# Kernel optimization log

Hardware: AMD Instinct MI355X
Metric: run time of the kernel (lower is better)

Reference implementation:

```python
import jax, jax.numpy as jnp
import numpy as np

L, N1, N2 = 2, 2, 2
E1 = sum(1 + i for i in range(N1))      # 3 first-stage DAG edges per layer
E2 = sum(N1 + i for i in range(N2))     # 5 last-stage DAG edges per layer
DIM, IN_DIM, NUM_CLASSES = 256, 128, 10
N_NODES, N_EDGES, N_GRAPHS = 8000, 128000, 64


def setup_inputs():
    key = jax.random.key(0)
    ks = jax.random.split(key, 16)
    s = 0.05  # weight scale to keep activations bounded through stacked cells
    return {
        'h': jax.random.normal(ks[0], (N_NODES, IN_DIM), jnp.float32),
        'W_emb': jax.random.normal(ks[1], (IN_DIM, DIM), jnp.float32) * s,
        'b_emb': jnp.zeros((DIM,), jnp.float32),
        'Wf_dense': jax.random.normal(ks[2], (L, E1, DIM, DIM), jnp.float32) * s,
        'bf_dense': jnp.zeros((L, E1, DIM), jnp.float32),
        'Wf_sparse': jax.random.normal(ks[3], (L, E1, DIM, DIM), jnp.float32) * s,
        'bf_sparse': jnp.zeros((L, E1, DIM), jnp.float32),
        'Wl_dense': jax.random.normal(ks[4], (L, E2, DIM, DIM), jnp.float32) * s,
        'bl_dense': jnp.zeros((L, E2, DIM), jnp.float32),
        'Wl_sparse': jax.random.normal(ks[5], (L, E2, DIM, DIM), jnp.float32) * s,
        'bl_sparse': jnp.zeros((L, E2, DIM), jnp.float32),
        'a_first': 0.001 * jax.random.normal(ks[6], (L * E1, 4), jnp.float32),
        'a_mid': 0.001 * jax.random.normal(ks[7], (L * N1, 4), jnp.float32),
        'a_last': 0.001 * jax.random.normal(ks[8], (L * E2, 4), jnp.float32),
        'C1': jax.random.normal(ks[9], (DIM, DIM // 2), jnp.float32) * s,
        'c1b': jnp.zeros((DIM // 2,), jnp.float32),
        'C2': jax.random.normal(ks[10], (DIM // 2, DIM // 4), jnp.float32) * s,
        'c2b': jnp.zeros((DIM // 4,), jnp.float32),
        'C3': jax.random.normal(ks[11], (DIM // 4, NUM_CLASSES), jnp.float32) * s,
        'c3b': jnp.zeros((NUM_CLASSES,), jnp.float32),
        'src': jax.random.randint(ks[12], (N_EDGES,), 0, N_NODES, jnp.int32),
        'dst': jax.random.randint(ks[13], (N_EDGES,), 0, N_NODES, jnp.int32),
        'graph_ids': jnp.sort(jax.random.randint(ks[14], (N_NODES,), 0, N_GRAPHS, jnp.int32)),
        'num_graphs': N_GRAPHS,
    }


def forward(h, W_emb, b_emb, Wf_dense, bf_dense, Wf_sparse, bf_sparse,
            Wl_dense, bl_dense, Wl_sparse, bl_sparse, a_first, a_mid, a_last,
            C1, c1b, C2, c2b, C3, c3b, src, dst, graph_ids, num_graphs):
    N = h.shape[0]
    deg0 = jax.ops.segment_sum(jnp.ones((src.shape[0],), h.dtype), dst, num_segments=N)
    deg = jnp.maximum(deg0, 1.0)[:, None]      # in-degree, clamped for mean
    has_nb = (deg0 > 0)[:, None]

    # DARTS softmax over candidate ops (per DAG edge)
    wf = jax.nn.softmax(a_first, axis=1)
    wm = jax.nn.softmax(a_mid, axis=1)
    wl = jax.nn.softmax(a_last, axis=1)

    def mixed(xj, w, Wd, bd, Ws, bs):
        # mixture over {f_zero, f_identity, f_dense, f_sparse}
        dense = xj @ Wd + bd
        agg = jax.ops.segment_sum(xj[src], dst, num_segments=N) / deg  # mean msg-passing
        sparse = agg @ Ws + bs
        return w[1] * xj + w[2] * dense + w[3] * sparse  # w[0]*zero omitted

    x = h @ W_emb + b_emb  # embedding (Linear, data_type='gc')
    for l in range(L):
        # first stage: DAG over N1 intermediate nodes
        states = [x]
        e = 0
        for n in range(1, N1 + 1):
            s = jnp.zeros_like(x)
            for j in range(n):
                s = s + mixed(states[j], wf[l * E1 + e], Wf_dense[l, e], bf_dense[l, e],
                              Wf_sparse[l, e], bf_sparse[l, e])
                e += 1
            states.append(jax.nn.relu(s))
        # middle stage: mixture over {identity, max, mean, sum} neighbor aggregators
        mids = []
        for n in range(N1):
            xn = states[n + 1]
            w = wm[l * N1 + n]
            msg = xn[src]
            msum = jax.ops.segment_sum(msg, dst, num_segments=N)
            mmean = msum / deg
            mmax = jnp.where(has_nb, jax.ops.segment_max(msg, dst, num_segments=N), 0.0)
            mids.append(w[0] * xn + w[1] * mmax + w[2] * mmean + w[3] * msum)
        # last stage: DAG over N2 output nodes, inputs = middle states + prior lasts
        lasts = []
        e = 0
        for n in range(N2):
            ins = mids + lasts
            s = jnp.zeros_like(x)
            for j in range(N1 + n):
                s = s + mixed(ins[j], wl[l * E2 + e], Wl_dense[l, e], bl_dense[l, e],
                              Wl_sparse[l, e], bl_sparse[l, e])
                e += 1
            lasts.append(jax.nn.relu(s))
        x = x + sum(lasts) / float(N2)  # residual cell output

    # dgl.mean_nodes readout: per-graph mean over nodes
    cnt = jnp.maximum(jax.ops.segment_sum(jnp.ones((N,), x.dtype), graph_ids,
                                          num_segments=num_graphs), 1.0)[:, None]
    hg = jax.ops.segment_sum(x, graph_ids, num_segments=num_graphs) / cnt
    # MLPReadout: 256 -> 128 -> 64 -> 10
    y = jax.nn.relu(hg @ C1 + c1b)
    y = jax.nn.relu(y @ C2 + c2b)
    return y @ C3 + c3b


def reference(h, W_emb, b_emb, Wf_dense, bf_dense, Wf_sparse, bf_sparse,
              Wl_dense, bl_dense, Wl_sparse, bl_sparse, a_first, a_mid, a_last,
              C1, c1b, C2, c2b, C3, c3b, src, dst, graph_ids, num_graphs):
    return forward(h, W_emb, b_emb, Wf_dense, bf_dense, Wf_sparse, bf_sparse,
                   Wl_dense, bl_dense, Wl_sparse, bl_sparse, a_first, a_mid, a_last,
                   C1, c1b, C2, c2b, C3, c3b, src, dst, graph_ids, num_graphs)
```

## Files before the change

### kernel.cpp

```cpp
#include <hip/hip_runtime.h>

#define N_NODES   8000
#define M_PAD     8192
#define N_EDGES   128000
#define N_GRAPHS  64
#define DIM       256
#define IN_DIM    128

typedef short bf16x8 __attribute__((ext_vector_type(8)));
typedef float f32x4 __attribute__((ext_vector_type(4)));

static __device__ __forceinline__ float bf2f(unsigned v) {
  return __uint_as_float(v << 16);
}
static __device__ __forceinline__ unsigned f2bf(float f) {
  unsigned u = __float_as_uint(f);
  return (u + 0x7fffu + ((u >> 16) & 1u)) >> 16;
}

__global__ __launch_bounds__(256) void k_count(const int* __restrict__ dst,
                                               int* __restrict__ counts) {
  int e = blockIdx.x * 256 + threadIdx.x;
  if (e < N_EDGES) atomicAdd(&counts[dst[e]], 1);
}

__global__ __launch_bounds__(256) void k_scan(const int* __restrict__ counts,
                                              int* __restrict__ row_ofs,
                                              int* __restrict__ cursor,
                                              float* __restrict__ invdeg) {
  __shared__ int chunk[256];
  const int per = (N_NODES + 255) / 256;
  int t = threadIdx.x;
  int base = t * per;
  int s = 0;
  for (int i = 0; i < per; ++i) {
    int idx = base + i;
    if (idx < N_NODES) s += counts[idx];
  }
  chunk[t] = s;
  __syncthreads();
  for (int off = 1; off < 256; off <<= 1) {
    int v = 0;
    if (t >= off) v = chunk[t - off];
    __syncthreads();
    if (t >= off) chunk[t] += v;
    __syncthreads();
  }
  int run = (t > 0) ? chunk[t - 1] : 0;
  for (int i = 0; i < per; ++i) {
    int idx = base + i;
    if (idx < N_NODES) {
      row_ofs[idx] = run;
      cursor[idx] = run;
      int c = counts[idx];
      invdeg[idx] = 1.0f / (float)(c > 1 ? c : 1);
      run += c;
    }
  }
  if (t == 0) row_ofs[N_NODES] = chunk[255];
}

__global__ __launch_bounds__(256) void k_fill(const int* __restrict__ src,
                                              const int* __restrict__ dst,
                                              int* __restrict__ cursor,
                                              int* __restrict__ csr_src) {
  int e = blockIdx.x * 256 + threadIdx.x;
  if (e < N_EDGES) {
    int p = atomicAdd(&cursor[dst[e]], 1);
    csr_src[p] = src[e];
  }
}

__global__ __launch_bounds__(64) void k_softmax(const float* __restrict__ af,
                                                const float* __restrict__ am,
                                                const float* __restrict__ al,
                                                float* __restrict__ w) {
  int t = threadIdx.x;
  const float* sp;
  float* dp;
  if (t < 6)       { sp = af + t * 4;        dp = w + t * 4; }
  else if (t < 10) { sp = am + (t - 6) * 4;  dp = w + 24 + (t - 6) * 4; }
  else if (t < 20) { sp = al + (t - 10) * 4; dp = w + 40 + (t - 10) * 4; }
  else return;
  float a0 = sp[0], a1 = sp[1], a2 = sp[2], a3 = sp[3];
  float m = fmaxf(fmaxf(a0, a1), fmaxf(a2, a3));
  float e0 = expf(a0 - m), e1 = expf(a1 - m), e2 = expf(a2 - m), e3 = expf(a3 - m);
  float si = 1.0f / (e0 + e1 + e2 + e3);
  dp[0] = e0 * si; dp[1] = e1 * si; dp[2] = e2 * si; dp[3] = e3 * si;
}

__global__ __launch_bounds__(256) void k_cvt_bf16(const float* __restrict__ in,
                                                  unsigned short* __restrict__ out,
                                                  int n) {
  int i = blockIdx.x * 256 + threadIdx.x;
  if (i < n) out[i] = (unsigned short)f2bf(in[i]);
}

__global__ __launch_bounds__(256) void k_transpose_cvt(const float* __restrict__ in,
                                                       unsigned short* __restrict__ out,
                                                       int K, int N) {
  __shared__ float tile[32][33];
  int k0 = blockIdx.x * 32, n0 = blockIdx.y * 32;
  int tx = threadIdx.x & 31, ty = threadIdx.x >> 5;
#pragma unroll
  for (int i = 0; i < 4; ++i)
    tile[ty + 8 * i][tx] = in[(size_t)(k0 + ty + 8 * i) * N + n0 + tx];
  __syncthreads();
#pragma unroll
  for (int i = 0; i < 4; ++i)
    out[(size_t)(n0 + ty + 8 * i) * K + k0 + tx] =
        (unsigned short)f2bf(tile[tx][ty + 8 * i]);
}

__global__ __launch_bounds__(256) void k_transpose_cvt32(const float* __restrict__ Wfd,
                                                         const float* __restrict__ Wfs,
                                                         const float* __restrict__ Wld,
                                                         const float* __restrict__ Wls,
                                                         const float* __restrict__ wsoft,
                                                         unsigned short* __restrict__ out) {
  __shared__ float tile[32][33];
  int z = blockIdx.z;
  const float* in;
  float coef;
  const float* wf = wsoft;
  const float* wl = wsoft + 40;
  if (z < 6)       { in = Wfd + (size_t)z * DIM * DIM;        coef = wf[z * 4 + 2]; }
  else if (z < 12) { in = Wfs + (size_t)(z - 6) * DIM * DIM;  coef = wf[(z - 6) * 4 + 3]; }
  else if (z < 22) { in = Wld + (size_t)(z - 12) * DIM * DIM; coef = wl[(z - 12) * 4 + 2]; }
  else             { in = Wls + (size_t)(z - 22) * DIM * DIM; coef = wl[(z - 22) * 4 + 3]; }
  unsigned short* o = out + (size_t)z * DIM * DIM;
  int k0 = blockIdx.x * 32, n0 = blockIdx.y * 32;
  int tx = threadIdx.x & 31, ty = threadIdx.x >> 5;
#pragma unroll
  for (int i = 0; i < 4; ++i)
    tile[ty + 8 * i][tx] = in[(size_t)(k0 + ty + 8 * i) * DIM + n0 + tx];
  __syncthreads();
#pragma unroll
  for (int i = 0; i < 4; ++i)
    o[(size_t)(n0 + ty + 8 * i) * DIM + k0 + tx] =
        (unsigned short)f2bf(coef * tile[tx][ty + 8 * i]);
}

#define SEG_ACC(u) \
  { s0 += bf2f((u).x & 0xffffu); s1 += bf2f((u).x >> 16); \
    s2 += bf2f((u).y & 0xffffu); s3 += bf2f((u).y >> 16); }

__global__ __launch_bounds__(256) void k_segmean_bf(const unsigned short* __restrict__ X,
                                                    const int* __restrict__ row_ofs,
                                                    const int* __restrict__ csr_src,
                                                    const float* __restrict__ invdeg,
                                                    unsigned short* __restrict__ out) {
  int node = blockIdx.x * 4 + (threadIdx.x >> 6);
  int l = threadIdx.x & 63;
  if (node >= N_NODES) return;
  int beg = row_ofs[node], end = row_ofs[node + 1];
  float s0 = 0.f, s1 = 0.f, s2 = 0.f, s3 = 0.f;
  int e = beg;
  for (; e + 4 <= end; e += 4) {
    int i0 = csr_src[e], i1 = csr_src[e + 1], i2 = csr_src[e + 2], i3 = csr_src[e + 3];
    uint2 u0 = *(const uint2*)&X[(size_t)i0 * DIM + 4 * l];
    uint2 u1 = *(const uint2*)&X[(size_t)i1 * DIM + 4 * l];
    uint2 u2 = *(const uint2*)&X[(size_t)i2 * DIM + 4 * l];
    uint2 u3 = *(const uint2*)&X[(size_t)i3 * DIM + 4 * l];
    SEG_ACC(u0) SEG_ACC(u1) SEG_ACC(u2) SEG_ACC(u3)
  }
  for (; e < end; ++e) {
    uint2 u = *(const uint2*)&X[(size_t)csr_src[e] * DIM + 4 * l];
    SEG_ACC(u)
  }
  float iv = invdeg[node];
  uint2 o;
  o.x = f2bf(s0 * iv) | (f2bf(s1 * iv) << 16);
  o.y = f2bf(s2 * iv) | (f2bf(s3 * iv) << 16);
  *(uint2*)&out[(size_t)node * DIM + 4 * l] = o;
}

__global__ __launch_bounds__(256) void k_segmean2_bf(const unsigned short* __restrict__ X0,
                                                     const unsigned short* __restrict__ X1,
                                                     const int* __restrict__ row_ofs,
                                                     const int* __restrict__ csr_src,
                                                     const float* __restrict__ invdeg,
                                                     unsigned short* __restrict__ out0,
                                                     unsigned short* __restrict__ out1) {
  int node = blockIdx.x * 4 + (threadIdx.x >> 6);
  int l = threadIdx.x & 63;
  if (node >= N_NODES) return;
  int beg = row_ofs[node], end = row_ofs[node + 1];
  float a0 = 0.f, a1 = 0.f, a2 = 0.f, a3 = 0.f;
  float b0 = 0.f, b1 = 0.f, b2 = 0.f, b3 = 0.f;
  int e = beg;
  for (; e + 2 <= end; e += 2) {
    size_t r0 = (size_t)csr_src[e] * DIM + 4 * l;
    size_t r1 = (size_t)csr_src[e + 1] * DIM + 4 * l;
    uint2 u0 = *(const uint2*)&X0[r0];
    uint2 v0 = *(const uint2*)&X1[r0];
    uint2 u1 = *(const uint2*)&X0[r1];
    uint2 v1 = *(const uint2*)&X1[r1];
    a0 += bf2f(u0.x & 0xffffu) + bf2f(u1.x & 0xffffu);
    a1 += bf2f(u0.x >> 16) + bf2f(u1.x >> 16);
    a2 += bf2f(u0.y & 0xffffu) + bf2f(u1.y & 0xffffu);
    a3 += bf2f(u0.y >> 16) + bf2f(u1.y >> 16);
    b0 += bf2f(v0.x & 0xffffu) + bf2f(v1.x & 0xffffu);
    b1 += bf2f(v0.x >> 16) + bf2f(v1.x >> 16);
    b2 += bf2f(v0.y & 0xffffu) + bf2f(v1.y & 0xffffu);
    b3 += bf2f(v0.y >> 16) + bf2f(v1.y >> 16);
  }
  for (; e < end; ++e) {
    size_t rb = (size_t)csr_src[e] * DIM + 4 * l;
    uint2 u = *(const uint2*)&X0[rb];
    uint2 v = *(const uint2*)&X1[rb];
    a0 += bf2f(u.x & 0xffffu); a1 += bf2f(u.x >> 16);
    a2 += bf2f(u.y & 0xffffu); a3 += bf2f(u.y >> 16);
    b0 += bf2f(v.x & 0xffffu); b1 += bf2f(v.x >> 16);
    b2 += bf2f(v.y & 0xffffu); b3 += bf2f(v.y >> 16);
  }
  float iv = invdeg[node];
  uint2 o;
  o.x = f2bf(a0 * iv) | (f2bf(a1 * iv) << 16);
  o.y = f2bf(a2 * iv) | (f2bf(a3 * iv) << 16);
  *(uint2*)&out0[(size_t)node * DIM + 4 * l] = o;
  o.x = f2bf(b0 * iv) | (f2bf(b1 * iv) << 16);
  o.y = f2bf(b2 * iv) | (f2bf(b3 * iv) << 16);
  *(uint2*)&out1[(size_t)node * DIM + 4 * l] = o;
}

__global__ __launch_bounds__(256) void k_segmid_bf(const unsigned short* __restrict__ Xn,
                                                   const int* __restrict__ row_ofs,
                                                   const int* __restrict__ csr_src,
                                                   const float* __restrict__ invdeg,
                                                   const float* __restrict__ wrow,
                                                   unsigned short* __restrict__ mean_out,
                                                   unsigned short* __restrict__ mids_out) {
  int node = blockIdx.x * 4 + (threadIdx.x >> 6);
  int l = threadIdx.x & 63;
  if (node >= N_NODES) return;
  int beg = row_ofs[node], end = row_ofs[node + 1];
  float s0 = 0.f, s1 = 0.f, s2 = 0.f, s3 = 0.f;
  float m0 = 0.f, m1 = 0.f, m2 = 0.f, m3 = 0.f;
  int e = beg;
  for (; e + 4 <= end; e += 4) {
    int i0 = csr_src[e], i1 = csr_src[e + 1], i2 = csr_src[e + 2], i3 = csr_src[e + 3];
    uint2 u0 = *(const uint2*)&Xn[(size_t)i0 * DIM + 4 * l];
    uint2 u1 = *(const uint2*)&Xn[(size_t)i1 * DIM + 4 * l];
    uint2 u2 = *(const uint2*)&Xn[(size_t)i2 * DIM + 4 * l];
    uint2 u3 = *(const uint2*)&Xn[(size_t)i3 * DIM + 4 * l];
#pragma unroll
    for (int j = 0; j < 4; ++j) {
      uint2 u = (j == 0) ? u0 : (j == 1) ? u1 : (j == 2) ? u2 : u3;
      float v0 = bf2f(u.x & 0xffffu), v1 = bf2f(u.x >> 16);
      float v2 = bf2f(u.y & 0xffffu), v3 = bf2f(u.y >> 16);
      s0 += v0; s1 += v1; s2 += v2; s3 += v3;
      m0 = fmaxf(m0, v0); m1 = fmaxf(m1, v1);
      m2 = fmaxf(m2, v2); m3 = fmaxf(m3, v3);
    }
  }
  for (; e < end; ++e) {
    uint2 u = *(const uint2*)&Xn[(size_t)csr_src[e] * DIM + 4 * l];
    float v0 = bf2f(u.x & 0xffffu), v1 = bf2f(u.x >> 16);
    float v2 = bf2f(u.y & 0xffffu), v3 = bf2f(u.y >> 16);
    s0 += v0; s1 += v1; s2 += v2; s3 += v3;
    m0 = fmaxf(m0, v0); m1 = fmaxf(m1, v1);
    m2 = fmaxf(m2, v2); m3 = fmaxf(m3, v3);
  }
  float iv = invdeg[node];
  float e0 = s0 * iv, e1 = s1 * iv, e2 = s2 * iv, e3 = s3 * iv;
  if (mean_out) {
    uint2 o;
    o.x = f2bf(e0) | (f2bf(e1) << 16);
    o.y = f2bf(e2) | (f2bf(e3) << 16);
    *(uint2*)&mean_out[(size_t)node * DIM + 4 * l] = o;
  }
  float w0 = wrow[0], w1 = wrow[1], w2 = wrow[2], w3 = wrow[3];
  uint2 xu = *(const uint2*)&Xn[(size_t)node * DIM + 4 * l];
  float x0 = bf2f(xu.x & 0xffffu), x1 = bf2f(xu.x >> 16);
  float x2 = bf2f(xu.y & 0xffffu), x3 = bf2f(xu.y >> 16);
  uint2 o;
  o.x = f2bf(w0 * x0 + w1 * m0 + w2 * e0 + w3 * s0) |
        (f2bf(w0 * x1 + w1 * m1 + w2 * e1 + w3 * s1) << 16);
  o.y = f2bf(w0 * x2 + w1 * m2 + w2 * e2 + w3 * s2) |
        (f2bf(w0 * x3 + w1 * m3 + w2 * e3 + w3 * s3) << 16);
  *(uint2*)&mids_out[(size_t)node * DIM + 4 * l] = o;
}

struct GemmDescB {
  const unsigned short* A[6];
  const unsigned short* W[6];
  const float* b[6];
  const float* c[6];
  const unsigned short* I[3];
  const float* ic[3];
  const float* resid;
  const unsigned short* addl;
  float* out_f32;
  unsigned short* out_bf;
  int nmat, nid, K, relu;
};

__global__ __launch_bounds__(256) void k_gemm_mfma(GemmDescB d) {
  __shared__ __align__(16) unsigned short As[2][64][72];
  __shared__ __align__(16) unsigned short Bs[2][64][72];
  const int tid = threadIdx.x;
  const int b = blockIdx.x;
  const int bm = ((b & 7) + 8 * (b >> 5)) * 64;
  const int bn = ((b >> 3) & 3) * 64;
  const int w = tid >> 6, l = tid & 63;
  const int wm = (w >> 1) * 32, wn = (w & 1) * 32;
  const int lr = l & 15, lk = (l >> 4) * 8;
  const int ldr = tid >> 3, ldk = (tid & 7) * 8;

  const int K = d.K;
  const int kds = (K == 256) ? 2 : 1;
  const int kmask = (1 << kds) - 1;
  const int nsteps = d.nmat << kds;

  f32x4 zero = {0.f, 0.f, 0.f, 0.f};
  f32x4 acc[2][2];
  acc[0][0] = zero; acc[0][1] = zero; acc[1][0] = zero; acc[1][1] = zero;

  auto gload = [&](int s, uint4& a0, uint4& a1, uint4& b0, uint4& b1) {
    int t = s >> kds;
    int k0 = (s & kmask) << 6;
    const unsigned short* __restrict__ A = d.A[t];
    const unsigned short* __restrict__ W = d.W[t];
    a0 = *(const uint4*)&A[(size_t)(bm + ldr) * K + k0 + ldk];
    a1 = *(const uint4*)&A[(size_t)(bm + ldr + 32) * K + k0 + ldk];
    b0 = *(const uint4*)&W[(size_t)(bn + ldr) * K + k0 + ldk];
    b1 = *(const uint4*)&W[(size_t)(bn + ldr + 32) * K + k0 + ldk];
  };

  {
    uint4 a0, a1, b0, b1;
    gload(0, a0, a1, b0, b1);
    *(uint4*)&As[0][ldr][ldk] = a0;
    *(uint4*)&As[0][ldr + 32][ldk] = a1;
    *(uint4*)&Bs[0][ldr][ldk] = b0;
    *(uint4*)&Bs[0][ldr + 32][ldk] = b1;
  }
  __syncthreads();

  int buf = 0;
  for (int s = 0; s < nsteps; ++s) {
    uint4 na0, na1, nb0, nb1;
    const bool more = (s + 1 < nsteps);
    if (more) gload(s + 1, na0, na1, nb0, nb1);
#pragma unroll
    for (int ks = 0; ks < 2; ++ks) {
      bf16x8 a0 = *(const bf16x8*)&As[buf][wm + lr][ks * 32 + lk];
      bf16x8 a1 = *(const bf16x8*)&As[buf][wm + 16 + lr][ks * 32 + lk];
      bf16x8 b0 = *(const bf16x8*)&Bs[buf][wn + lr][ks * 32 + lk];
      bf16x8 b1 = *(const bf16x8*)&Bs[buf][wn + 16 + lr][ks * 32 + lk];
      acc[0][0] = __builtin_amdgcn_mfma_f32_16x16x32_bf16(a0, b0, acc[0][0], 0, 0, 0);
      acc[0][1] = __builtin_amdgcn_mfma_f32_16x16x32_bf16(a0, b1, acc[0][1], 0, 0, 0);
      acc[1][0] = __builtin_amdgcn_mfma_f32_16x16x32_bf16(a1, b0, acc[1][0], 0, 0, 0);
      acc[1][1] = __builtin_amdgcn_mfma_f32_16x16x32_bf16(a1, b1, acc[1][1], 0, 0, 0);
    }
    if (more) {
      *(uint4*)&As[buf ^ 1][ldr][ldk] = na0;
      *(uint4*)&As[buf ^ 1][ldr + 32][ldk] = na1;
      *(uint4*)&Bs[buf ^ 1][ldr][ldk] = nb0;
      *(uint4*)&Bs[buf ^ 1][ldr + 32][ldk] = nb1;
    }
    __syncthreads();
    buf ^= 1;
  }

  float bias[2] = {0.f, 0.f};
  for (int t = 0; t < d.nmat; ++t) {
    if (d.b[t]) {
      float c = d.c[t] ? *d.c[t] : 1.0f;
      bias[0] += c * d.b[t][bn + wn + lr];
      bias[1] += c * d.b[t][bn + wn + 16 + lr];
    }
  }
  float vout[2][2][4];
#pragma unroll
  for (int m = 0; m < 2; ++m)
#pragma unroll
    for (int n = 0; n < 2; ++n)
#pragma unroll
      for (int i = 0; i < 4; ++i) vout[m][n][i] = acc[m][n][i] + bias[n];
#pragma unroll
  for (int u = 0; u < 3; ++u) {
    if (u < d.nid) {
      float icu = *d.ic[u];
      const unsigned short* __restrict__ I = d.I[u];
#pragma unroll
      for (int m = 0; m < 2; ++m)
#pragma unroll
        for (int n = 0; n < 2; ++n)
#pragma unroll
          for (int i = 0; i < 4; ++i) {
            int row = bm + wm + m * 16 + (l >> 4) * 4 + i;
            int col = bn + wn + n * 16 + lr;
            vout[m][n][i] += icu * bf2f(I[(size_t)row * DIM + col]);
          }
    }
  }
#pragma unroll
  for (int m = 0; m < 2; ++m)
#pragma unroll
    for (int n = 0; n < 2; ++n)
#pragma unroll
      for (int i = 0; i < 4; ++i) {
        int row = bm + wm + m * 16 + (l >> 4) * 4 + i;
        int col = bn + wn + n * 16 + lr;
        size_t idx = (size_t)row * DIM + col;
        float v = vout[m][n][i];
        if (d.relu) v = fmaxf(v, 0.f);
        if (d.resid) v = d.resid[idx] + 0.5f * (bf2f(d.addl[idx]) + v);
        d.out_bf[idx] = (unsigned short)f2bf(v);
        if (d.out_f32) d.out_f32[idx] = v;
      }
}

__global__ __launch_bounds__(256) void k_readout(const float* __restrict__ x,
                                                 const int* __restrict__ gid,
                                                 float* __restrict__ hg) {
  int g = blockIdx.x, t = threadIdx.x;
  int lo = 0, hi = N_NODES;
  while (lo < hi) { int m = (lo + hi) >> 1; if (gid[m] < g) lo = m + 1; else hi = m; }
  int beg = lo;
  lo = beg; hi = N_NODES;
  while (lo < hi) { int m = (lo + hi) >> 1; if (gid[m] <= g) lo = m + 1; else hi = m; }
  int end = lo;
  float s = 0.f;
  for (int i = beg; i < end; ++i) s += x[(size_t)i * DIM + t];
  int cnt = end - beg;
  hg[g * DIM + t] = s / (float)(cnt > 1 ? cnt : 1);
}

__global__ __launch_bounds__(256) void k_mlp(const float* __restrict__ hg,
                                             const float* __restrict__ C1,
                                             const float* __restrict__ c1b,
                                             const float* __restrict__ C2,
                                             const float* __restrict__ c2b,
                                             const float* __restrict__ C3,
                                             const float* __restrict__ c3b,
                                             float* __restrict__ out) {
  int g = blockIdx.x, t = threadIdx.x;
  __shared__ float h0[256], h1[128], h2[64];
  h0[t] = hg[g * DIM + t];
  __syncthreads();
  if (t < 128) {
    float s = c1b[t];
    for (int k = 0; k < 256; ++k) s = fmaf(h0[k], C1[k * 128 + t], s);
    h1[t] = fmaxf(s, 0.f);
  }
  __syncthreads();
  if (t < 64) {
    float s = c2b[t];
    for (int k = 0; k < 128; ++k) s = fmaf(h1[k], C2[k * 64 + t], s);
    h2[t] = fmaxf(s, 0.f);
  }
  __syncthreads();
  if (t < 10) {
    float s = c3b[t];
    for (int k = 0; k < 64; ++k) s = fmaf(h2[k], C3[k * 10 + t], s);
    out[g * 10 + t] = s;
  }
}

extern "C" void kernel_launch(void* const* d_in, const int* in_sizes, int n_in,
                              void* d_out, int out_size, void* d_ws, size_t ws_size,
                              hipStream_t stream) {
  const float* h     = (const float*)d_in[0];
  const float* W_emb = (const float*)d_in[1];
  const float* b_emb = (const float*)d_in[2];
  const float* Wf_d  = (const float*)d_in[3];
  const float* bf_d  = (const float*)d_in[4];
  const float* Wf_s  = (const float*)d_in[5];
  const float* bf_s  = (const float*)d_in[6];
  const float* Wl_d  = (const float*)d_in[7];
  const float* bl_d  = (const float*)d_in[8];
  const float* Wl_s  = (const float*)d_in[9];
  const float* bl_s  = (const float*)d_in[10];
  const float* a_first = (const float*)d_in[11];
  const float* a_mid   = (const float*)d_in[12];
  const float* a_last  = (const float*)d_in[13];
  const float* C1 = (const float*)d_in[14];
  const float* c1b = (const float*)d_in[15];
  const float* C2 = (const float*)d_in[16];
  const float* c2b = (const float*)d_in[17];
  const float* C3 = (const float*)d_in[18];
  const float* c3b = (const float*)d_in[19];
  const int* src = (const int*)d_in[20];
  const int* dst = (const int*)d_in[21];
  const int* gid = (const int*)d_in[22];
  (void)in_sizes; (void)n_in; (void)out_size; (void)ws_size;

  char* p = (char*)d_ws;
  auto alloc = [&](size_t bytes) {
    void* r = (void*)p;
    p += (bytes + 255) & ~(size_t)255;
    return r;
  };
  typedef unsigned short u16;
  const size_t NBF = (size_t)M_PAD * DIM * sizeof(u16);
  float* x_f32 = (float*)alloc((size_t)M_PAD * DIM * sizeof(float));
  u16* xb    = (u16*)alloc(NBF);
  u16* s1b   = (u16*)alloc(NBF);
  u16* s2b   = (u16*)alloc(NBF);
  u16* m0b   = (u16*)alloc(NBF);
  u16* m1b   = (u16*)alloc(NBF);
  u16* l0b   = (u16*)alloc(NBF);
  u16* aggAb = (u16*)alloc(NBF);
  u16* aggBb = (u16*)alloc(NBF);
  u16* h_bf  = (u16*)alloc((size_t)M_PAD * IN_DIM * sizeof(u16));
  u16* WT    = (u16*)alloc((size_t)(DIM * IN_DIM + 32 * DIM * DIM) * sizeof(u16));
  u16* WTe   = WT;
  u16* WTfd  = WT + DIM * IN_DIM;
  u16* WTfs  = WTfd + 6 * DIM * DIM;
  u16* WTld  = WTfs + 6 * DIM * DIM;
  u16* WTls  = WTld + 10 * DIM * DIM;
  float* invdeg = (float*)alloc(N_NODES * sizeof(float));
  int* counts  = (int*)alloc(N_NODES * sizeof(int));
  int* row_ofs = (int*)alloc((N_NODES + 1) * sizeof(int));
  int* cursor  = (int*)alloc(N_NODES * sizeof(int));
  int* csr_src = (int*)alloc(N_EDGES * sizeof(int));
  float* wsoft = (float*)alloc(80 * sizeof(float));
  float* hg    = (float*)alloc(N_GRAPHS * DIM * sizeof(float));

  const int EB = (N_EDGES + 255) / 256;
  const int PADR = M_PAD - N_NODES;

  hipMemsetAsync(counts, 0, N_NODES * sizeof(int), stream);
  hipMemsetAsync(h_bf + (size_t)N_NODES * IN_DIM, 0, (size_t)PADR * IN_DIM * sizeof(u16), stream);
  hipMemsetAsync(aggAb + (size_t)N_NODES * DIM, 0, (size_t)PADR * DIM * sizeof(u16), stream);
  hipMemsetAsync(aggBb + (size_t)N_NODES * DIM, 0, (size_t)PADR * DIM * sizeof(u16), stream);
  hipMemsetAsync(m0b + (size_t)N_NODES * DIM, 0, (size_t)PADR * DIM * sizeof(u16), stream);
  hipMemsetAsync(m1b + (size_t)N_NODES * DIM, 0, (size_t)PADR * DIM * sizeof(u16), stream);

  k_count<<<EB, 256, 0, stream>>>(dst, counts);
  k_scan<<<1, 256, 0, stream>>>(counts, row_ofs, cursor, invdeg);
  k_fill<<<EB, 256, 0, stream>>>(src, dst, cursor, csr_src);
  k_softmax<<<1, 64, 0, stream>>>(a_first, a_mid, a_last, wsoft);

  const float* wf = wsoft;
  const float* wm = wsoft + 24;
  const float* wl = wsoft + 40;

  k_cvt_bf16<<<(N_NODES * IN_DIM + 255) / 256, 256, 0, stream>>>(h, h_bf, N_NODES * IN_DIM);
  k_transpose_cvt<<<dim3(IN_DIM / 32, DIM / 32, 1), 256, 0, stream>>>(W_emb, WTe, IN_DIM, DIM);
  k_transpose_cvt32<<<dim3(8, 8, 32), 256, 0, stream>>>(Wf_d, Wf_s, Wl_d, Wl_s, wsoft, WTfd);

  const int GG = (M_PAD / 64) * (DIM / 64);
  const int SB = (N_NODES + 3) / 4;

  {
    GemmDescB d{};
    d.A[0] = h_bf; d.W[0] = WTe; d.b[0] = b_emb; d.c[0] = nullptr;
    d.nmat = 1; d.nid = 0; d.K = IN_DIM; d.relu = 0;
    d.out_f32 = x_f32; d.out_bf = xb;
    k_gemm_mfma<<<GG, 256, 0, stream>>>(d);
  }

  for (int l = 0; l < 2; ++l) {
    auto WFD = [&](int e) { return WTfd + (size_t)(l * 3 + e) * DIM * DIM; };
    auto BFD = [&](int e) { return bf_d + (size_t)(l * 3 + e) * DIM; };
    auto WFS = [&](int e) { return WTfs + (size_t)(l * 3 + e) * DIM * DIM; };
    auto BFS = [&](int e) { return bf_s + (size_t)(l * 3 + e) * DIM; };
    auto WLD = [&](int e) { return WTld + (size_t)(l * 5 + e) * DIM * DIM; };
    auto BLD = [&](int e) { return bl_d + (size_t)(l * 5 + e) * DIM; };
    auto WLS = [&](int e) { return WTls + (size_t)(l * 5 + e) * DIM * DIM; };
    auto BLS = [&](int e) { return bl_s + (size_t)(l * 5 + e) * DIM; };
    auto WFrow = [&](int e) { return wf + (l * 3 + e) * 4; };
    auto WMrow = [&](int n) { return wm + (l * 2 + n) * 4; };
    auto WLrow = [&](int e) { return wl + (l * 5 + e) * 4; };

    auto edge = [&](GemmDescB& d, const u16* X, const u16* AG,
                    const u16* Wd, const float* bd,
                    const u16* Ws, const float* bs, const float* wrow) {
      d.A[d.nmat] = X;  d.W[d.nmat] = Wd; d.b[d.nmat] = bd; d.c[d.nmat] = wrow + 2; d.nmat++;
      d.A[d.nmat] = AG; d.W[d.nmat] = Ws; d.b[d.nmat] = bs; d.c[d.nmat] = wrow + 3; d.nmat++;
      d.I[d.nid] = X; d.ic[d.nid] = wrow + 1; d.nid++;
    };

    k_segmean_bf<<<SB, 256, 0, stream>>>(xb, row_ofs, csr_src, invdeg, aggAb);

    {
      GemmDescB d{}; d.K = DIM; d.relu = 1; d.out_bf = s1b;
      edge(d, xb, aggAb, WFD(0), BFD(0), WFS(0), BFS(0), WFrow(0));
      k_gemm_mfma<<<GG, 256, 0, stream>>>(d);
    }

    k_segmid_bf<<<SB, 256, 0, stream>>>(s1b, row_ofs, csr_src, invdeg, WMrow(0), aggBb, m0b);

    {
      GemmDescB d{}; d.K = DIM; d.relu = 1; d.out_bf = s2b;
      edge(d, xb,  aggAb, WFD(1), BFD(1), WFS(1), BFS(1), WFrow(1));
      edge(d, s1b, aggBb, WFD(2), BFD(2), WFS(2), BFS(2), WFrow(2));
      k_gemm_mfma<<<GG, 256, 0, stream>>>(d);
    }

    k_segmid_bf<<<SB, 256, 0, stream>>>(s2b, row_ofs, csr_src, invdeg, WMrow(1), nullptr, m1b);

    k_segmean2_bf<<<SB, 256, 0, stream>>>(m0b, m1b, row_ofs, csr_src, invdeg, aggAb, aggBb);

    {
      GemmDescB d{}; d.K = DIM; d.relu = 1; d.out_bf = l0b;
      edge(d, m0b, aggAb, WLD(0), BLD(0), WLS(0), BLS(0), WLrow(0));
      edge(d, m1b, aggBb, WLD(1), BLD(1), WLS(1), BLS(1), WLrow(1));
      k_gemm_mfma<<<GG, 256, 0, stream>>>(d);
    }

    k_segmean_bf<<<SB, 256, 0, stream>>>(l0b, row_ofs, csr_src, invdeg, s1b);

    {
      GemmDescB d{}; d.K = DIM; d.relu = 1;
      edge(d, m0b, aggAb, WLD(2), BLD(2), WLS(2), BLS(2), WLrow(2));
      edge(d, m1b, aggBb, WLD(3), BLD(3), WLS(3), BLS(3), WLrow(3));
      edge(d, l0b, s1b,   WLD(4), BLD(4), WLS(4), BLS(4), WLrow(4));
      d.resid = x_f32; d.addl = l0b;
      d.out_f32 = x_f32; d.out_bf = xb;
      k_gemm_mfma<<<GG, 256, 0, stream>>>(d);
    }
  }

  k_readout<<<N_GRAPHS, 256, 0, stream>>>(x_f32, gid, hg);
  k_mlp<<<N_GRAPHS, 256, 0, stream>>>(hg, C1, c1b, C2, c2b, C3, c3b, (float*)d_out);
}
```

Before: 361.3 us.

## Share A-operand loads across sibling edge GEMMs via wide-N dual-output tiles

The GEMM kernel can now produce two output halves, each with its own weights, bias and epilogue. Edges that read the same inputs (xb/aggA for first-stage edges 0 and 1, m0/m1 for last-stage edges 0-3) are computed in one wider launch, with the partial sum saved in fp32 and added back later through a new 'pre' term. This stops the later GEMMs from re-reading the shared operands and shrinks their K depth. The cost is extra fp32 partial buffers written and read back. The separate memsets are also merged into a single init kernel.

Result: no change. 359.7 us (-0.4%).

```diff
diff --git a/kernel.cpp b/kernel.cpp
--- a/kernel.cpp
+++ b/kernel.cpp
@@ -2,6 +2,7 @@
 
 #define N_NODES   8000
 #define M_PAD     8192
+#define PADR      (M_PAD - N_NODES)
 #define N_EDGES   128000
 #define N_GRAPHS  64
 #define DIM       256
@@ -16,6 +17,18 @@
 static __device__ __forceinline__ unsigned f2bf(float f) {
   unsigned u = __float_as_uint(f);
   return (u + 0x7fffu + ((u >> 16) & 1u)) >> 16;
+}
+
+__global__ __launch_bounds__(256) void k_init(int* __restrict__ counts,
+                                              unsigned short* __restrict__ hpad,
+                                              unsigned short* __restrict__ p0,
+                                              unsigned short* __restrict__ p1,
+                                              unsigned short* __restrict__ p2,
+                                              unsigned short* __restrict__ p3) {
+  int i = blockIdx.x * 256 + threadIdx.x;
+  if (i < N_NODES) counts[i] = 0;
+  if (i < PADR * IN_DIM) hpad[i] = 0;
+  if (i < PADR * DIM) { p0[i] = 0; p1[i] = 0; p2[i] = 0; p3[i] = 0; }
 }
 
 __global__ __launch_bounds__(256) void k_count(const int* __restrict__ dst,
@@ -282,27 +295,31 @@
   *(uint2*)&mids_out[(size_t)node * DIM + 4 * l] = o;
 }
 
-struct GemmDescB {
-  const unsigned short* A[6];
-  const unsigned short* W[6];
-  const float* b[6];
-  const float* c[6];
-  const unsigned short* I[3];
-  const float* ic[3];
-  const float* resid;
-  const unsigned short* addl;
-  float* out_f32;
-  unsigned short* out_bf;
-  int nmat, nid, K, relu;
+struct GemmDescW {
+  const unsigned short* A[4];
+  const unsigned short* W[2][4];
+  const float* b[2][4];
+  const float* c[2][4];
+  const unsigned short* I[2];
+  const float* ic[2][2];
+  const float* pre[2];
+  const float* resid[2];
+  const unsigned short* addl[2];
+  float* out_f32[2];
+  unsigned short* out_bf[2];
+  int nmat, nid, K, relu[2], colshift;
 };
 
-__global__ __launch_bounds__(256) void k_gemm_mfma(GemmDescB d) {
+__global__ __launch_bounds__(256) void k_gemm_mfma(GemmDescW d) {
   __shared__ __align__(16) unsigned short As[2][64][72];
   __shared__ __align__(16) unsigned short Bs[2][64][72];
   const int tid = threadIdx.x;
   const int b = blockIdx.x;
-  const int bm = ((b & 7) + 8 * (b >> 5)) * 64;
-  const int bn = ((b >> 3) & 3) * 64;
+  const int cs = d.colshift;
+  const int c = (b >> 3) & ((1 << cs) - 1);
+  const int bm = ((b & 7) + 8 * (b >> (3 + cs))) * 64;
+  const int half = c >> 2;
+  const int bn = (c & 3) * 64;
   const int w = tid >> 6, l = tid & 63;
   const int wm = (w >> 1) * 32, wn = (w & 1) * 32;
   const int lr = l & 15, lk = (l >> 4) * 8;
@@ -321,7 +338,7 @@
     int t = s >> kds;
     int k0 = (s & kmask) << 6;
     const unsigned short* __restrict__ A = d.A[t];
-    const unsigned short* __restrict__ W = d.W[t];
+    const unsigned short* __restrict__ W = d.W[half][t];
     a0 = *(const uint4*)&A[(size_t)(bm + ldr) * K + k0 + ldk];
     a1 = *(const uint4*)&A[(size_t)(bm + ldr + 32) * K + k0 + ldk];
     b0 = *(const uint4*)&W[(size_t)(bn + ldr) * K + k0 + ldk];
@@ -366,10 +383,11 @@
 
   float bias[2] = {0.f, 0.f};
   for (int t = 0; t < d.nmat; ++t) {
-    if (d.b[t]) {
-      float c = d.c[t] ? *d.c[t] : 1.0f;
-      bias[0] += c * d.b[t][bn + wn + lr];
-      bias[1] += c * d.b[t][bn + wn + 16 + lr];
+    const float* bp = d.b[half][t];
+    if (bp) {
+      float cc = d.c[half][t] ? *d.c[half][t] : 1.0f;
+      bias[0] += cc * bp[bn + wn + lr];
+      bias[1] += cc * bp[bn + wn + 16 + lr];
     }
   }
   float vout[2][2][4];
@@ -380,9 +398,9 @@
 #pragma unroll
       for (int i = 0; i < 4; ++i) vout[m][n][i] = acc[m][n][i] + bias[n];
 #pragma unroll
-  for (int u = 0; u < 3; ++u) {
+  for (int u = 0; u < 2; ++u) {
     if (u < d.nid) {
-      float icu = *d.ic[u];
+      float icu = *d.ic[half][u];
       const unsigned short* __restrict__ I = d.I[u];
 #pragma unroll
       for (int m = 0; m < 2; ++m)
@@ -396,6 +414,12 @@
           }
     }
   }
+  const float* pre = d.pre[half];
+  const float* resid = d.resid[half];
+  const unsigned short* addl = d.addl[half];
+  unsigned short* obf = d.out_bf[half];
+  float* of32 = d.out_f32[half];
+  const int do_relu = d.relu[half];
 #pragma unroll
   for (int m = 0; m < 2; ++m)
 #pragma unroll
@@ -406,10 +430,11 @@
         int col = bn + wn + n * 16 + lr;
         size_t idx = (size_t)row * DIM + col;
         float v = vout[m][n][i];
-        if (d.relu) v = fmaxf(v, 0.f);
-        if (d.resid) v = d.resid[idx] + 0.5f * (bf2f(d.addl[idx]) + v);
-        d.out_bf[idx] = (unsigned short)f2bf(v);
-        if (d.out_f32) d.out_f32[idx] = v;
+        if (pre) v += pre[idx];
+        if (do_relu) v = fmaxf(v, 0.f);
+        if (resid) v = resid[idx] + 0.5f * (bf2f(addl[idx]) + v);
+        if (obf) obf[idx] = (unsigned short)f2bf(v);
+        if (of32) of32[idx] = v;
       }
 }
 
@@ -496,7 +521,9 @@
   };
   typedef unsigned short u16;
   const size_t NBF = (size_t)M_PAD * DIM * sizeof(u16);
-  float* x_f32 = (float*)alloc((size_t)M_PAD * DIM * sizeof(float));
+  float* x_f32  = (float*)alloc((size_t)M_PAD * DIM * sizeof(float));
+  float* s2part = (float*)alloc((size_t)M_PAD * DIM * sizeof(float));
+  float* xpart  = (float*)alloc((size_t)M_PAD * DIM * sizeof(float));
   u16* xb    = (u16*)alloc(NBF);
   u16* s1b   = (u16*)alloc(NBF);
   u16* s2b   = (u16*)alloc(NBF);
@@ -521,14 +548,11 @@
   float* hg    = (float*)alloc(N_GRAPHS * DIM * sizeof(float));
 
   const int EB = (N_EDGES + 255) / 256;
-  const int PADR = M_PAD - N_NODES;
-
-  hipMemsetAsync(counts, 0, N_NODES * sizeof(int), stream);
-  hipMemsetAsync(h_bf + (size_t)N_NODES * IN_DIM, 0, (size_t)PADR * IN_DIM * sizeof(u16), stream);
-  hipMemsetAsync(aggAb + (size_t)N_NODES * DIM, 0, (size_t)PADR * DIM * sizeof(u16), stream);
-  hipMemsetAsync(aggBb + (size_t)N_NODES * DIM, 0, (size_t)PADR * DIM * sizeof(u16), stream);
-  hipMemsetAsync(m0b + (size_t)N_NODES * DIM, 0, (size_t)PADR * DIM * sizeof(u16), stream);
-  hipMemsetAsync(m1b + (size_t)N_NODES * DIM, 0, (size_t)PADR * DIM * sizeof(u16), stream);
+
+  k_init<<<(PADR * DIM + 255) / 256 > 32 ? (PADR * DIM + 255) / 256 : 32, 256, 0, stream>>>(
+      counts, h_bf + (size_t)N_NODES * IN_DIM,
+      aggAb + (size_t)N_NODES * DIM, aggBb + (size_t)N_NODES * DIM,
+      m0b + (size_t)N_NODES * DIM, m1b + (size_t)N_NODES * DIM);
 
   k_count<<<EB, 256, 0, stream>>>(dst, counts);
   k_scan<<<1, 256, 0, stream>>>(counts, row_ofs, cursor, invdeg);
@@ -543,15 +567,16 @@
   k_transpose_cvt<<<dim3(IN_DIM / 32, DIM / 32, 1), 256, 0, stream>>>(W_emb, WTe, IN_DIM, DIM);
   k_transpose_cvt32<<<dim3(8, 8, 32), 256, 0, stream>>>(Wf_d, Wf_s, Wl_d, Wl_s, wsoft, WTfd);
 
-  const int GG = (M_PAD / 64) * (DIM / 64);
+  const int GG1 = (M_PAD / 64) * 4;
+  const int GG2 = (M_PAD / 64) * 8;
   const int SB = (N_NODES + 3) / 4;
 
   {
-    GemmDescB d{};
-    d.A[0] = h_bf; d.W[0] = WTe; d.b[0] = b_emb; d.c[0] = nullptr;
-    d.nmat = 1; d.nid = 0; d.K = IN_DIM; d.relu = 0;
-    d.out_f32 = x_f32; d.out_bf = xb;
-    k_gemm_mfma<<<GG, 256, 0, stream>>>(d);
+    GemmDescW d{};
+    d.A[0] = h_bf; d.W[0][0] = WTe; d.b[0][0] = b_emb;
+    d.nmat = 1; d.nid = 0; d.K = IN_DIM; d.colshift = 2;
+    d.out_f32[0] = x_f32; d.out_bf[0] = xb;
+    k_gemm_mfma<<<GG1, 256, 0, stream>>>(d);
   }
 
   for (int l = 0; l < 2; ++l) {
@@ -567,29 +592,31 @@
     auto WMrow = [&](int n) { return wm + (l * 2 + n) * 4; };
     auto WLrow = [&](int e) { return wl + (l * 5 + e) * 4; };
 
-    auto edge = [&](GemmDescB& d, const u16* X, const u16* AG,
-                    const u16* Wd, const float* bd,
-                    const u16* Ws, const float* bs, const float* wrow) {
-      d.A[d.nmat] = X;  d.W[d.nmat] = Wd; d.b[d.nmat] = bd; d.c[d.nmat] = wrow + 2; d.nmat++;
-      d.A[d.nmat] = AG; d.W[d.nmat] = Ws; d.b[d.nmat] = bs; d.c[d.nmat] = wrow + 3; d.nmat++;
-      d.I[d.nid] = X; d.ic[d.nid] = wrow + 1; d.nid++;
-    };
-
     k_segmean_bf<<<SB, 256, 0, stream>>>(xb, row_ofs, csr_src, invdeg, aggAb);
 
     {
-      GemmDescB d{}; d.K = DIM; d.relu = 1; d.out_bf = s1b;
-      edge(d, xb, aggAb, WFD(0), BFD(0), WFS(0), BFS(0), WFrow(0));
-      k_gemm_mfma<<<GG, 256, 0, stream>>>(d);
+      GemmDescW d{};
+      d.A[0] = xb; d.A[1] = aggAb; d.nmat = 2; d.K = DIM; d.colshift = 3;
+      d.I[0] = xb; d.nid = 1;
+      d.W[0][0] = WFD(0); d.b[0][0] = BFD(0); d.c[0][0] = WFrow(0) + 2;
+      d.W[0][1] = WFS(0); d.b[0][1] = BFS(0); d.c[0][1] = WFrow(0) + 3;
+      d.ic[0][0] = WFrow(0) + 1; d.relu[0] = 1; d.out_bf[0] = s1b;
+      d.W[1][0] = WFD(1); d.b[1][0] = BFD(1); d.c[1][0] = WFrow(1) + 2;
+      d.W[1][1] = WFS(1); d.b[1][1] = BFS(1); d.c[1][1] = WFrow(1) + 3;
+      d.ic[1][0] = WFrow(1) + 1; d.relu[1] = 0; d.out_f32[1] = s2part;
+      k_gemm_mfma<<<GG2, 256, 0, stream>>>(d);
     }
 
     k_segmid_bf<<<SB, 256, 0, stream>>>(s1b, row_ofs, csr_src, invdeg, WMrow(0), aggBb, m0b);
 
     {
-      GemmDescB d{}; d.K = DIM; d.relu = 1; d.out_bf = s2b;
-      edge(d, xb,  aggAb, WFD(1), BFD(1), WFS(1), BFS(1), WFrow(1));
-      edge(d, s1b, aggBb, WFD(2), BFD(2), WFS(2), BFS(2), WFrow(2));
-      k_gemm_mfma<<<GG, 256, 0, stream>>>(d);
+      GemmDescW d{};
+      d.A[0] = s1b; d.A[1] = aggBb; d.nmat = 2; d.K = DIM; d.colshift = 2;
+      d.I[0] = s1b; d.nid = 1;
+      d.W[0][0] = WFD(2); d.b[0][0] = BFD(2); d.c[0][0] = WFrow(2) + 2;
+      d.W[0][1] = WFS(2); d.b[0][1] = BFS(2); d.c[0][1] = WFrow(2) + 3;
+      d.ic[0][0] = WFrow(2) + 1; d.pre[0] = s2part; d.relu[0] = 1; d.out_bf[0] = s2b;
+      k_gemm_mfma<<<GG1, 256, 0, stream>>>(d);
     }
 
     k_segmid_bf<<<SB, 256, 0, stream>>>(s2b, row_ofs, csr_src, invdeg, WMrow(1), nullptr, m1b);
@@ -597,22 +624,37 @@
     k_segmean2_bf<<<SB, 256, 0, stream>>>(m0b, m1b, row_ofs, csr_src, invdeg, aggAb, aggBb);
 
     {
-      GemmDescB d{}; d.K = DIM; d.relu = 1; d.out_bf = l0b;
-      edge(d, m0b, aggAb, WLD(0), BLD(0), WLS(0), BLS(0), WLrow(0));
-      edge(d, m1b, aggBb, WLD(1), BLD(1), WLS(1), BLS(1), WLrow(1));
-      k_gemm_mfma<<<GG, 256, 0, stream>>>(d);
+      GemmDescW d{};
+      d.A[0] = m0b; d.A[1] = aggAb; d.A[2] = m1b; d.A[3] = aggBb;
+      d.nmat = 4; d.K = DIM; d.colshift = 3;
+      d.I[0] = m0b; d.I[1] = m1b; d.nid = 2;
+      d.W[0][0] = WLD(0); d.b[0][0] = BLD(0); d.c[0][0] = WLrow(0) + 2;
+      d.W[0][1] = WLS(0); d.b[0][1] = BLS(0); d.c[0][1] = WLrow(0) + 3;
+      d.W[0][2] = WLD(1); d.b[0][2] = BLD(1); d.c[0][2] = WLrow(1) + 2;
+      d.W[0][3] = WLS(1); d.b[0][3] = BLS(1); d.c[0][3] = WLrow(1) + 3;
+      d.ic[0][0] = WLrow(0) + 1; d.ic[0][1] = WLrow(1) + 1;
+      d.relu[0] = 1; d.out_bf[0] = l0b;
+      d.W[1][0] = WLD(2); d.b[1][0] = BLD(2); d.c[1][0] = WLrow(2) + 2;
+      d.W[1][1] = WLS(2); d.b[1][1] = BLS(2); d.c[1][1] = WLrow(2) + 3;
+      d.W[1][2] = WLD(3); d.b[1][2] = BLD(3); d.c[1][2] = WLrow(3) + 2;
+      d.W[1][3] = WLS(3); d.b[1][3] = BLS(3); d.c[1][3] = WLrow(3) + 3;
+      d.ic[1][0] = WLrow(2) + 1; d.ic[1][1] = WLrow(3) + 1;
+      d.relu[1] = 0; d.out_f32[1] = xpart;
+      k_gemm_mfma<<<GG2, 256, 0, stream>>>(d);
     }
 
     k_segmean_bf<<<SB, 256, 0, stream>>>(l0b, row_ofs, csr_src, invdeg, s1b);
 
     {
-      GemmDescB d{}; d.K = DIM; d.relu = 1;
-      edge(d, m0b, aggAb, WLD(2), BLD(2), WLS(2), BLS(2), WLrow(2));
-      edge(d, m1b, aggBb, WLD(3), BLD(3), WLS(3), BLS(3), WLrow(3));
-      edge(d, l0b, s1b,   WLD(4), BLD(4), WLS(4), BLS(4), WLrow(4));
-      d.resid = x_f32; d.addl = l0b;
-      d.out_f32 = x_f32; d.out_bf = xb;
-      k_gemm_mfma<<<GG, 256, 0, stream>>>(d);
+      GemmDescW d{};
+      d.A[0] = l0b; d.A[1] = s1b; d.nmat = 2; d.K = DIM; d.colshift = 2;
+      d.I[0] = l0b; d.nid = 1;
+      d.W[0][0] = WLD(4); d.b[0][0] = BLD(4); d.c[0][0] = WLrow(4) + 2;
+      d.W[0][1] = WLS(4); d.b[0][1] = BLS(4); d.c[0][1] = WLrow(4) + 3;
+      d.ic[0][0] = WLrow(4) + 1; d.pre[0] = xpart; d.relu[0] = 1;
+      d.resid[0] = x_f32; d.addl[0] = l0b;
+      d.out_f32[0] = x_f32; d.out_bf[0] = xb;
+      k_gemm_mfma<<<GG1, 256, 0, stream>>>(d);
     }
   }
 
```
